# Kernel optimization log

Hardware: AMD Instinct MI355X
Metric: run time of the kernel (lower is better)

Reference implementation:

```python
import jax, jax.numpy as jnp
import numpy as np
import math

B, T, C = 4, 2048, 2048
HQ, HKV = 16, 4
HD = C // HQ          # 128
REP = HQ // HKV       # 4
EPS = 1e-6


def _rope_tables(seq_len, dim):
    inv_freq = 1.0 / (10000.0 ** (np.arange(0, dim, 2, dtype=np.float32) / dim))
    t = np.arange(seq_len, dtype=np.float32)
    freqs = np.einsum('i,j->ij', t, inv_freq)  # [T, dim/2]
    return jnp.asarray(np.cos(freqs)), jnp.asarray(np.sin(freqs))


def setup_inputs() -> dict:
    key = jax.random.key(0)
    ks = jax.random.split(key, 10)
    s = 0.02
    cos, sin = _rope_tables(T, HD)
    return {
        'x': jax.random.normal(ks[0], (B, T, C), jnp.float32),
        'Wq': jax.random.normal(ks[1], (C, C), jnp.float32) * s,
        'bq': jnp.zeros((C,), jnp.float32),
        'Wk': jax.random.normal(ks[2], (HD * HKV, C), jnp.float32) * s,
        'bk': jnp.zeros((HD * HKV,), jnp.float32),
        'Wv': jax.random.normal(ks[3], (HD * HKV, C), jnp.float32) * s,
        'bv': jnp.zeros((HD * HKV,), jnp.float32),
        'qn_w': jnp.ones((HD,), jnp.float32),
        'kn_w': jnp.ones((HD,), jnp.float32),
        'Wg': jax.random.normal(ks[4], (HD, HD), jnp.float32) * s,
        'bg': jnp.zeros((HD,), jnp.float32),
        'Wo': jax.random.normal(ks[5], (C, C), jnp.float32) * s,
        'bo': jnp.zeros((C,), jnp.float32),
        'cos': cos,
        'sin': sin,
    }


def _apply_rope(x, cos, sin):
    # x: [B,T,H,HD]; cos/sin: [T,HD/2]
    c = cos[None, :, None, :]
    s = sin[None, :, None, :]
    x1, x2 = x[..., ::2], x[..., 1::2]
    return jnp.concatenate([x1 * c - x2 * s, x1 * s + x2 * c], axis=-1)


def _rmsnorm(x, w):
    norm = jnp.mean(x * x, axis=-1, keepdims=True)
    return w * (x * jax.lax.rsqrt(norm + EPS))


def reference(x, Wq, bq, Wk, bk, Wv, bv, qn_w, kn_w, Wg, bg, Wo, bo, cos, sin):
    Bsz, Tlen, _ = x.shape
    q = (x @ Wq.T + bq).reshape(Bsz, Tlen, HQ, HD)
    k = (x @ Wk.T + bk).reshape(Bsz, Tlen, HKV, HD)
    v = (x @ Wv.T + bv).reshape(Bsz, Tlen, HKV, HD)

    q = _rmsnorm(_apply_rope(q, cos, sin), qn_w)
    k = _rmsnorm(_apply_rope(k, cos, sin), kn_w)

    # GQA without materializing repeated K/V: group q heads [B,T,HKV,REP,HD]
    # (repeat_interleave on kv-head dim matches this grouping exactly)
    q5 = q.reshape(Bsz, Tlen, HKV, REP, HD)
    scores = jnp.einsum('btkrd,bskd->bkrts', q5, k) / math.sqrt(HD)

    causal = jnp.tril(jnp.ones((Tlen, Tlen), bool))
    scores = jnp.where(causal, scores, -jnp.inf)
    probs = jax.nn.softmax(scores, axis=-1)

    out = jnp.einsum('bkrts,bskd->btkrd', probs, v).reshape(Bsz, Tlen, HQ, HD)
    gate = jax.nn.sigmoid(out @ Wg.T + bg)
    out = (out * gate).reshape(Bsz, Tlen, C)
    return out @ Wo.T + bo
```

## Files before the change

### kernel.cpp

```cpp
#include <hip/hip_runtime.h>
#include <hip/hip_bf16.h>
#include <math.h>

typedef __attribute__((ext_vector_type(8))) __bf16 bf16x8;
typedef __attribute__((ext_vector_type(4))) float f32x4;

__device__ __forceinline__ void stage16(const void* g, void* l) {
#if __has_builtin(__builtin_amdgcn_global_load_lds)
  __builtin_amdgcn_global_load_lds(
      (const __attribute__((address_space(1))) void*)g,
      (__attribute__((address_space(3))) void*)l, 16, 0, 0);
#else
  *(int4*)l = *(const int4*)g;
#endif
}

__device__ __forceinline__ float sigmoidf_(float x) {
  return 1.0f / (1.0f + __expf(-x));
}

__device__ __forceinline__ void f2b4(const float* __restrict__ s, __bf16* __restrict__ d) {
  float4 v = *(const float4*)s;
  union { __bf16 h[4]; int2 p; } u;
  u.h[0] = (__bf16)v.x; u.h[1] = (__bf16)v.y;
  u.h[2] = (__bf16)v.z; u.h[3] = (__bf16)v.w;
  *(int2*)d = u.p;
}

__global__ __launch_bounds__(256) void prep(const float* __restrict__ x,
                                            const float* __restrict__ Wq,
                                            const float* __restrict__ Wk,
                                            const float* __restrict__ Wv,
                                            const float* __restrict__ Wo,
                                            const float* __restrict__ Wg,
                                            const float* __restrict__ bq,
                                            const float* __restrict__ bk,
                                            const float* __restrict__ bv,
                                            __bf16* __restrict__ XB,
                                            __bf16* __restrict__ WQKVb,
                                            __bf16* __restrict__ WOb,
                                            __bf16* __restrict__ WGb,
                                            float* __restrict__ BQKV) {
  int c = blockIdx.x * 256 + threadIdx.x;
  if (c >= 6820608) return;
  if (c < 4194304) {
    f2b4(x + (size_t)c * 4, XB + (size_t)c * 4);
  } else if (c < 5242880) {
    int e = (c - 4194304) * 4;  f2b4(Wq + e, WQKVb + e);
  } else if (c < 5505024) {
    int e = (c - 5242880) * 4;  f2b4(Wk + e, WQKVb + 4194304 + e);
  } else if (c < 5767168) {
    int e = (c - 5505024) * 4;  f2b4(Wv + e, WQKVb + 5242880 + e);
  } else if (c < 6815744) {
    int e = (c - 5767168) * 4;  f2b4(Wo + e, WOb + e);
  } else if (c < 6819840) {
    int e = (c - 6815744) * 4;  f2b4(Wg + e, WGb + e);
  } else {
    int e = (c - 6819840) * 4;
    float4 v;
    if (e < 2048)      v = *(const float4*)(bq + e);
    else if (e < 2560) v = *(const float4*)(bk + (e - 2048));
    else               v = *(const float4*)(bv + (e - 2560));
    *(float4*)(BQKV + e) = v;
  }
}

template <typename OutT>
__global__ __launch_bounds__(512, 1) void gemm256(const __bf16* __restrict__ A,
                                                  const __bf16* __restrict__ Bm,
                                                  const float* __restrict__ bias,
                                                  OutT* __restrict__ C,
                                                  int M, int N, int K, int gx) {
  __shared__ __align__(16) __bf16 Sm[2][2][2][128 * 64];
  const int tid = threadIdx.x, lane = tid & 63, wid = tid >> 6;
  const int wm = wid >> 2, wn = wid & 3;
  const int r = lane & 15, g4 = lane >> 4;
  const int nwg = gridDim.x, qx = nwg >> 3;
  const int wg = (blockIdx.x & 7) * qx + (blockIdx.x >> 3);
  const int m0 = (wg / gx) * 256, n0 = (wg % gx) * 256;

  f32x4 acc[8][4] = {};
  const int NT = K >> 6;

#define STAGE_HALF(buf, which, half, kt)                                          \
  {                                                                               \
    const __bf16* sp_ = (which) ? Bm : A;                                         \
    const int base_ = ((which) ? n0 : m0) + (half) * 128;                         \
    const int k0_ = (kt) << 6;                                                    \
    __bf16* dp_ = &Sm[buf][which][half][0];                                       \
    _Pragma("unroll") for (int i_ = 0; i_ < 2; ++i_) {                            \
      int c_ = i_ * 512 + tid;                                                    \
      int row_ = c_ >> 3, slot_ = c_ & 7;                                         \
      stage16(sp_ + (size_t)(base_ + row_) * K + k0_ + ((slot_ ^ (row_ & 7)) << 3), \
              dp_ + c_ * 8);                                                      \
    }                                                                             \
  }
#define LDSW(base, row, kk) \
  (*(const bf16x8*)&(base)[(row) * 64 + ((((kk) * 4 + g4) ^ ((row) & 7)) << 3)])

  STAGE_HALF(0, 0, 0, 0) STAGE_HALF(0, 0, 1, 0) STAGE_HALF(0, 1, 0, 0) STAGE_HALF(0, 1, 1, 0)

  const int brow = (wn & 1) * 64;
  bf16x8 af[4][2], bfr[2][2];

  for (int kt = 0; kt < NT; ++kt) {
    const int cur = kt & 1, nxt = cur ^ 1;
    const bool more = (kt + 1) < NT;
    const __bf16* Ah = &Sm[cur][0][wm][0];
    const __bf16* Bh = &Sm[cur][1][wn >> 1][0];

    if (more) STAGE_HALF(nxt, 0, 0, kt + 1)
    if (more) { asm volatile("s_waitcnt vmcnt(2)" ::: "memory"); }
    else      { asm volatile("s_waitcnt vmcnt(0)" ::: "memory"); }
    __builtin_amdgcn_s_barrier();
    asm volatile("" ::: "memory");
#pragma unroll
    for (int m = 0; m < 4; ++m)
#pragma unroll
      for (int kk = 0; kk < 2; ++kk) af[m][kk] = LDSW(Ah, m * 16 + r, kk);
#pragma unroll
    for (int n = 0; n < 2; ++n)
#pragma unroll
      for (int kk = 0; kk < 2; ++kk) bfr[n][kk] = LDSW(Bh, brow + n * 16 + r, kk);
    asm volatile("s_waitcnt lgkmcnt(0)" ::: "memory");
    __builtin_amdgcn_sched_barrier(0);
    __builtin_amdgcn_s_setprio(1);
#pragma unroll
    for (int m = 0; m < 4; ++m)
#pragma unroll
      for (int n = 0; n < 2; ++n)
#pragma unroll
        for (int kk = 0; kk < 2; ++kk)
          acc[m][n] = __builtin_amdgcn_mfma_f32_16x16x32_bf16(af[m][kk], bfr[n][kk],
                                                              acc[m][n], 0, 0, 0);
    __builtin_amdgcn_s_setprio(0);
    __builtin_amdgcn_s_barrier();

#pragma unroll
    for (int n = 0; n < 2; ++n)
#pragma unroll
      for (int kk = 0; kk < 2; ++kk) bfr[n][kk] = LDSW(Bh, brow + (2 + n) * 16 + r, kk);
    if (more) STAGE_HALF(nxt, 0, 1, kt + 1)
    asm volatile("s_waitcnt lgkmcnt(0)" ::: "memory");
    __builtin_amdgcn_sched_barrier(0);
    __builtin_amdgcn_s_setprio(1);
#pragma unroll
    for (int m = 0; m < 4; ++m)
#pragma unroll
      for (int n = 0; n < 2; ++n)
#pragma unroll
        for (int kk = 0; kk < 2; ++kk)
          acc[m][2 + n] = __builtin_amdgcn_mfma_f32_16x16x32_bf16(af[m][kk], bfr[n][kk],
                                                                  acc[m][2 + n], 0, 0, 0);
    __builtin_amdgcn_s_setprio(0);
    __builtin_amdgcn_s_barrier();

#pragma unroll
    for (int m = 0; m < 4; ++m)
#pragma unroll
      for (int kk = 0; kk < 2; ++kk) af[m][kk] = LDSW(Ah, (4 + m) * 16 + r, kk);
#pragma unroll
    for (int n = 0; n < 2; ++n)
#pragma unroll
      for (int kk = 0; kk < 2; ++kk) bfr[n][kk] = LDSW(Bh, brow + n * 16 + r, kk);
    if (more) STAGE_HALF(nxt, 1, 0, kt + 1)
    asm volatile("s_waitcnt lgkmcnt(0)" ::: "memory");
    __builtin_amdgcn_sched_barrier(0);
    __builtin_amdgcn_s_setprio(1);
#pragma unroll
    for (int m = 0; m < 4; ++m)
#pragma unroll
      for (int n = 0; n < 2; ++n)
#pragma unroll
        for (int kk = 0; kk < 2; ++kk)
          acc[4 + m][n] = __builtin_amdgcn_mfma_f32_16x16x32_bf16(af[m][kk], bfr[n][kk],
                                                                  acc[4 + m][n], 0, 0, 0);
    __builtin_amdgcn_s_setprio(0);
    __builtin_amdgcn_s_barrier();

#pragma unroll
    for (int n = 0; n < 2; ++n)
#pragma unroll
      for (int kk = 0; kk < 2; ++kk) bfr[n][kk] = LDSW(Bh, brow + (2 + n) * 16 + r, kk);
    if (more) STAGE_HALF(nxt, 1, 1, kt + 1)
    asm volatile("s_waitcnt lgkmcnt(0)" ::: "memory");
    __builtin_amdgcn_sched_barrier(0);
    __builtin_amdgcn_s_setprio(1);
#pragma unroll
    for (int m = 0; m < 4; ++m)
#pragma unroll
      for (int n = 0; n < 2; ++n)
#pragma unroll
        for (int kk = 0; kk < 2; ++kk)
          acc[4 + m][2 + n] = __builtin_amdgcn_mfma_f32_16x16x32_bf16(af[m][kk], bfr[n][kk],
                                                                      acc[4 + m][2 + n], 0, 0, 0);
    __builtin_amdgcn_s_setprio(0);
    __builtin_amdgcn_s_barrier();
  }

  const int rq = lane >> 4;
#pragma unroll
  for (int m = 0; m < 8; ++m)
#pragma unroll
    for (int n = 0; n < 4; ++n) {
      int col = n0 + wn * 64 + n * 16 + r;
      float bv = bias ? bias[col] : 0.0f;
#pragma unroll
      for (int j = 0; j < 4; ++j) {
        int row = m0 + wm * 128 + m * 16 + rq * 4 + j;
        C[(size_t)row * N + col] = (OutT)(acc[m][n][j] + bv);
      }
    }
#undef STAGE_HALF
#undef LDSW
}

__global__ __launch_bounds__(512, 1) void gemm128(const __bf16* __restrict__ A,
                                                  const __bf16* __restrict__ Bm,
                                                  const float* __restrict__ bias,
                                                  __bf16* __restrict__ C,
                                                  int M, int N, int K, int gx) {
  __shared__ __align__(16) __bf16 Sm[2][3][128 * 64];
  const int tid = threadIdx.x, lane = tid & 63, wid = tid >> 6;
  const int wm = wid >> 2, wn = wid & 3;
  const int r = lane & 15, g4 = lane >> 4;
  const int nwg = gridDim.x, qx = nwg >> 3;
  const int wg = (blockIdx.x & 7) * qx + (blockIdx.x >> 3);
  const int m0 = (wg / gx) * 128, n0 = (wg % gx) * 256;

  f32x4 acc[4][4] = {};
  const int NT = K >> 6;

#define STAGE_SEG(buf, seg, sp, rowbase, kt)                                        \
  {                                                                                 \
    __bf16* dp_ = &Sm[buf][seg][0];                                                 \
    const int k0_ = (kt) << 6;                                                      \
    _Pragma("unroll") for (int i_ = 0; i_ < 2; ++i_) {                              \
      int c_ = i_ * 512 + tid;                                                      \
      int row_ = c_ >> 3, slot_ = c_ & 7;                                           \
      stage16((sp) + (size_t)((rowbase) + row_) * K + k0_ + ((slot_ ^ (row_ & 7)) << 3), \
              dp_ + c_ * 8);                                                        \
    }                                                                               \
  }
#define LDSW(base, row, kk) \
  (*(const bf16x8*)&(base)[(row) * 64 + ((((kk) * 4 + g4) ^ ((row) & 7)) << 3)])

  STAGE_SEG(0, 0, A, m0, 0) STAGE_SEG(0, 1, Bm, n0, 0) STAGE_SEG(0, 2, Bm, n0 + 128, 0)

  const int bseg = 1 + (wn >> 1);
  const int brow = (wn & 1) * 64;
  bf16x8 af[4][2], bfr[2][2];

  for (int kt = 0; kt < NT; ++kt) {
    const int cur = kt & 1, nxt = cur ^ 1;
    const bool more = (kt + 1) < NT;
    const __bf16* Ah = &Sm[cur][0][0];
    const __bf16* Bh = &Sm[cur][bseg][0];

    if (more) { STAGE_SEG(nxt, 0, A, m0, kt + 1) STAGE_SEG(nxt, 1, Bm, n0, kt + 1) }
    if (more) { asm volatile("s_waitcnt vmcnt(4)" ::: "memory"); }
    else      { asm volatile("s_waitcnt vmcnt(0)" ::: "memory"); }
    __builtin_amdgcn_s_barrier();
    asm volatile("" ::: "memory");
#pragma unroll
    for (int m = 0; m < 4; ++m)
#pragma unroll
      for (int kk = 0; kk < 2; ++kk) af[m][kk] = LDSW(Ah, wm * 64 + m * 16 + r, kk);
#pragma unroll
    for (int n = 0; n < 2; ++n)
#pragma unroll
      for (int kk = 0; kk < 2; ++kk) bfr[n][kk] = LDSW(Bh, brow + n * 16 + r, kk);
    asm volatile("s_waitcnt lgkmcnt(0)" ::: "memory");
    __builtin_amdgcn_sched_barrier(0);
    __builtin_amdgcn_s_setprio(1);
#pragma unroll
    for (int m = 0; m < 4; ++m)
#pragma unroll
      for (int n = 0; n < 2; ++n)
#pragma unroll
        for (int kk = 0; kk < 2; ++kk)
          acc[m][n] = __builtin_amdgcn_mfma_f32_16x16x32_bf16(af[m][kk], bfr[n][kk],
                                                              acc[m][n], 0, 0, 0);
    __builtin_amdgcn_s_setprio(0);
    __builtin_amdgcn_s_barrier();

#pragma unroll
    for (int n = 0; n < 2; ++n)
#pragma unroll
      for (int kk = 0; kk < 2; ++kk) bfr[n][kk] = LDSW(Bh, brow + (2 + n) * 16 + r, kk);
    if (more) STAGE_SEG(nxt, 2, Bm, n0 + 128, kt + 1)
    asm volatile("s_waitcnt lgkmcnt(0)" ::: "memory");
    __builtin_amdgcn_sched_barrier(0);
    __builtin_amdgcn_s_setprio(1);
#pragma unroll
    for (int m = 0; m < 4; ++m)
#pragma unroll
      for (int n = 0; n < 2; ++n)
#pragma unroll
        for (int kk = 0; kk < 2; ++kk)
          acc[m][2 + n] = __builtin_amdgcn_mfma_f32_16x16x32_bf16(af[m][kk], bfr[n][kk],
                                                                  acc[m][2 + n], 0, 0, 0);
    __builtin_amdgcn_s_setprio(0);
    __builtin_amdgcn_s_barrier();
  }

  const int rq = lane >> 4;
#pragma unroll
  for (int m = 0; m < 4; ++m)
#pragma unroll
    for (int n = 0; n < 4; ++n) {
      int col = n0 + wn * 64 + n * 16 + r;
      float bv = bias ? bias[col] : 0.0f;
#pragma unroll
      for (int j = 0; j < 4; ++j) {
        int row = m0 + wm * 64 + m * 16 + rq * 4 + j;
        C[(size_t)row * N + col] = (__bf16)(acc[m][n][j] + bv);
      }
    }
#undef STAGE_SEG
#undef LDSW
}

__global__ __launch_bounds__(256) void rope_vt(const __bf16* __restrict__ Y,
                                               const float* __restrict__ cosT,
                                               const float* __restrict__ sinT,
                                               const float* __restrict__ qn,
                                               const float* __restrict__ kn,
                                               __bf16* __restrict__ qat,
                                               __bf16* __restrict__ kat,
                                               __bf16* __restrict__ VT) {
  __shared__ __bf16 tile[32][66];
  if (blockIdx.x < 8192) {
    const int tok = blockIdx.x;
    const int b = tok >> 11, t = tok & 2047;
    const int wv = threadIdx.x >> 6, l = threadIdx.x & 63;
    const __bf16* row = Y + (size_t)tok * 3072;
    const float c = cosT[t * 64 + l], s = sinT[t * 64 + l];
    const float QS = 0.08838834764831845f * 1.4426950408889634f;
#pragma unroll
    for (int i = 0; i < 5; ++i) {
      const int h = wv + i * 4;
      const bool isq = h < 16;
      const int base = isq ? h * 128 : 2048 + (h - 16) * 128;
      union { uint32_t u; __bf16 h2[2]; } p;
      p.u = *(const uint32_t*)(row + base + 2 * l);
      float x1 = (float)p.h2[0], x2 = (float)p.h2[1];
      float v1 = x1 * c - x2 * s;
      float v2 = x1 * s + x2 * c;
      float ss = v1 * v1 + v2 * v2;
#pragma unroll
      for (int o = 32; o >= 1; o >>= 1) ss += __shfl_xor(ss, o, 64);
      float rms = rsqrtf(ss * (1.0f / 128.0f) + 1e-6f);
      if (isq) rms *= QS;
      float w1 = isq ? qn[l] : kn[l];
      float w2 = isq ? qn[64 + l] : kn[64 + l];
      size_t ob = isq ? (((size_t)b * 16 + h) * 2048 + t) * 128
                      : (((size_t)b * 4 + (h - 16)) * 2048 + t) * 128;
      __bf16* dst = isq ? qat : kat;
      dst[ob + l] = (__bf16)(w1 * v1 * rms);
      dst[ob + 64 + l] = (__bf16)(w2 * v2 * rms);
    }
  } else {
    const int i = blockIdx.x - 8192;
    const int t0 = (i & 31) * 64;
    const int d0 = ((i >> 5) & 3) * 32;
    const int bh = i >> 7;
    const int b = bh >> 2, hv = bh & 3;
    const __bf16* src = Y + (size_t)b * 2048 * 3072 + 2560 + hv * 128 + d0;
    const int dd = threadIdx.x & 31, tt = threadIdx.x >> 5;
#pragma unroll
    for (int p = 0; p < 8; ++p) {
      int t = tt + p * 8;
      tile[dd][t] = src[(size_t)(t0 + t) * 3072 + dd];
    }
    __syncthreads();
    __bf16* dst = VT + ((size_t)bh * 128 + d0) * 2048 + t0;
    const int oc = threadIdx.x & 63, orr = threadIdx.x >> 6;
#pragma unroll
    for (int p = 0; p < 8; ++p) {
      int d = orr + p * 4;
      dst[(size_t)d * 2048 + oc] = tile[d][oc];
    }
  }
}

__global__ __launch_bounds__(512, 4) void attn9(const __bf16* __restrict__ Q,
                                                const __bf16* __restrict__ Kg,
                                                const __bf16* __restrict__ VTg,
                                                __bf16* __restrict__ ab) {
  __shared__ __align__(16) __bf16 Kt[2][64 * 128];
  __shared__ __align__(16) __bf16 Vt[2][128 * 64];
  __shared__ __align__(16) __bf16 Ps[8 * 16 * 64];
  const int tid = threadIdx.x, lane = tid & 63, wv = tid >> 6;
  const int L = blockIdx.x;
  const int xcd = L & 7, slot = L >> 3;
  const int group = xcd * 2 + (slot >> 5);
  const int idx = slot & 31;
  const int b = group >> 2, hkv = group & 3;
  const int hq = hkv * 4 + (idx >> 3);
  const int p = idx & 7;
  const __bf16* qp = Q + ((size_t)b * 16 + hq) * 2048 * 128;
  const __bf16* kp = Kg + ((size_t)b * 4 + hkv) * 2048 * 128;
  const __bf16* vp = VTg + ((size_t)b * 4 + hkv) * 128 * 2048;
  const int r = lane & 15, g4 = lane >> 4, ks = g4 * 8;

  bf16x8 vone;
#pragma unroll
  for (int e = 0; e < 8; ++e) vone[e] = (__bf16)1.0f;

#define STAGE_TILE(bi, kv0)                                                  \
  {                                                                          \
    __bf16* Kb = &Kt[bi][0];                                                 \
    __bf16* Vb = &Vt[bi][0];                                                 \
    _Pragma("unroll") for (int i = 0; i < 2; ++i) {                          \
      int c = i * 512 + tid;                                                 \
      int row = c >> 4, slot_ = c & 15;                                      \
      int gco = ((slot_ ^ (row & 7)) << 3);                                  \
      stage16(kp + (size_t)((kv0) + row) * 128 + gco, &Kb[c * 8]);           \
    }                                                                        \
    _Pragma("unroll") for (int i = 0; i < 2; ++i) {                          \
      int c = i * 512 + tid;                                                 \
      int row = c >> 3, slot_ = c & 7;                                       \
      int gco = ((slot_ ^ (row & 7)) << 3);                                  \
      stage16(vp + (size_t)row * 2048 + (kv0) + gco, &Vb[c * 8]);            \
    }                                                                        \
  }

  for (int half = 0; half < 2; ++half) {
    const int qt = half == 0 ? (15 - p) : p;
    const int q0 = qt * 128 + wv * 16;

    bf16x8 qf[4];
#pragma unroll
    for (int kk = 0; kk < 4; ++kk)
      qf[kk] = *(const bf16x8*)(qp + (size_t)(q0 + r) * 128 + kk * 32 + ks);

    f32x4 Of[8] = {};
    f32x4 Lacc = {};
    float mrow[4] = {-1e30f, -1e30f, -1e30f, -1e30f};

    const int nt = 2 * qt + 2;
    STAGE_TILE(0, 0);
    int cur = 0;
    for (int t = 0; t < nt; ++t) {
      const int kv0 = t * 64;
      if (t + 1 < nt) {
        STAGE_TILE(cur ^ 1, (t + 1) * 64);
        asm volatile("s_waitcnt vmcnt(4)" ::: "memory");
      } else {
        asm volatile("s_waitcnt vmcnt(0)" ::: "memory");
      }
      __builtin_amdgcn_s_barrier();

      const __bf16* Kb = &Kt[cur][0];
      const __bf16* Vb = &Vt[cur][0];

      f32x4 s[4];
      __builtin_amdgcn_s_setprio(1);
#pragma unroll
      for (int kj = 0; kj < 4; ++kj) {
        f32x4 sa = {};
        int krow = kj * 16 + r;
#pragma unroll
        for (int kk = 0; kk < 4; ++kk) {
          int slot_ = (kk * 4 + g4) ^ (r & 7);
          bf16x8 kf = *(const bf16x8*)&Kb[krow * 128 + slot_ * 8];
          sa = __builtin_amdgcn_mfma_f32_16x16x32_bf16(qf[kk], kf, sa, 0, 0, 0);
        }
        s[kj] = sa;
      }
      __builtin_amdgcn_s_setprio(0);
      if (kv0 + 63 > q0) {
#pragma unroll
        for (int kj = 0; kj < 4; ++kj)
#pragma unroll
          for (int j = 0; j < 4; ++j) {
            int kv = kv0 + kj * 16 + r;
            int qrow = q0 + g4 * 4 + j;
            if (kv > qrow) s[kj][j] = -1e30f;
          }
      }
      float tm[4];
#pragma unroll
      for (int j = 0; j < 4; ++j)
        tm[j] = fmaxf(fmaxf(s[0][j], s[1][j]), fmaxf(s[2][j], s[3][j]));
      bool need = (tm[0] > mrow[0] + 8.0f) | (tm[1] > mrow[1] + 8.0f) |
                  (tm[2] > mrow[2] + 8.0f) | (tm[3] > mrow[3] + 8.0f);
      if (__any(need)) {
#pragma unroll
        for (int o = 8; o >= 1; o >>= 1)
#pragma unroll
          for (int j = 0; j < 4; ++j) tm[j] = fmaxf(tm[j], __shfl_xor(tm[j], o, 64));
#pragma unroll
        for (int j = 0; j < 4; ++j) {
          float mn = fmaxf(mrow[j], tm[j]);
          float corr = exp2f(mrow[j] - mn);
          mrow[j] = mn;
          Lacc[j] *= corr;
#pragma unroll
          for (int f = 0; f < 8; ++f) Of[f][j] *= corr;
        }
      }
#pragma unroll
      for (int kj = 0; kj < 4; ++kj)
#pragma unroll
        for (int j = 0; j < 4; ++j) s[kj][j] = exp2f(s[kj][j] - mrow[j]);

      __bf16* pw = &Ps[wv * 16 * 64];
#pragma unroll
      for (int kj = 0; kj < 4; ++kj)
#pragma unroll
        for (int j = 0; j < 4; ++j) {
          int qr = g4 * 4 + j;
          int kvl = kj * 16 + r;
          int sl = (kvl >> 3) ^ (qr & 7);
          pw[qr * 64 + sl * 8 + (kvl & 7)] = (__bf16)s[kj][j];
        }
      __builtin_amdgcn_s_setprio(1);
#pragma unroll
      for (int kvj = 0; kvj < 2; ++kvj) {
        int sl = (kvj * 4 + g4) ^ (r & 7);
        bf16x8 pa = *(const bf16x8*)&pw[r * 64 + sl * 8];
        Lacc = __builtin_amdgcn_mfma_f32_16x16x32_bf16(pa, vone, Lacc, 0, 0, 0);
#pragma unroll
        for (int dn = 0; dn < 8; ++dn) {
          bf16x8 vb = *(const bf16x8*)&Vb[(dn * 16 + r) * 64 + sl * 8];
          Of[dn] = __builtin_amdgcn_mfma_f32_16x16x32_bf16(pa, vb, Of[dn], 0, 0, 0);
        }
      }
      __builtin_amdgcn_s_setprio(0);
      __builtin_amdgcn_s_barrier();
      cur ^= 1;
    }

    float inv[4];
#pragma unroll
    for (int j = 0; j < 4; ++j) inv[j] = 1.0f / Lacc[j];
#pragma unroll
    for (int dn = 0; dn < 8; ++dn)
#pragma unroll
      for (int j = 0; j < 4; ++j) {
        int row = q0 + g4 * 4 + j;
        int d = dn * 16 + r;
        ab[(((size_t)b * 2048 + row) * 16 + hq) * 128 + d] = (__bf16)(Of[dn][j] * inv[j]);
      }
  }
#undef STAGE_TILE
}

__global__ __launch_bounds__(256) void gate_fused(const __bf16* __restrict__ a,
                                                  const __bf16* __restrict__ WgB,
                                                  const float* __restrict__ bg,
                                                  __bf16* __restrict__ og) {
  __shared__ __align__(16) __bf16 Wl[128 * 128];
  const int tid = threadIdx.x, lane = tid & 63, wv = tid >> 6;
  const int r = lane & 15, g4 = lane >> 4, ks = g4 * 8;
#pragma unroll
  for (int i = 0; i < 8; ++i) {
    int c = i * 256 + tid;
    int row = c >> 4, slot = c & 15;
    *(bf16x8*)&Wl[row * 128 + ((slot ^ (row & 7)) << 3)] =
        *(const bf16x8*)&WgB[row * 128 + slot * 8];
  }
  __syncthreads();
  const size_t r0 = (size_t)blockIdx.x * 64 + wv * 16;
  bf16x8 af[4];
#pragma unroll
  for (int kk = 0; kk < 4; ++kk)
    af[kk] = *(const bf16x8*)(a + (r0 + r) * 128 + kk * 32 + ks);
  f32x4 acc[8] = {};
#pragma unroll
  for (int dn = 0; dn < 8; ++dn) {
    int row = dn * 16 + r;
#pragma unroll
    for (int kk = 0; kk < 4; ++kk) {
      bf16x8 bf_ = *(const bf16x8*)&Wl[row * 128 + (((kk * 4 + g4) ^ (row & 7)) << 3)];
      acc[dn] = __builtin_amdgcn_mfma_f32_16x16x32_bf16(af[kk], bf_, acc[dn], 0, 0, 0);
    }
  }
#pragma unroll
  for (int dn = 0; dn < 8; ++dn) {
    float bgv = bg[dn * 16 + r];
#pragma unroll
    for (int j = 0; j < 4; ++j) {
      size_t row = r0 + g4 * 4 + j;
      int col = dn * 16 + r;
      float gv = sigmoidf_(acc[dn][j] + bgv);
      float av = (float)a[row * 128 + col];
      og[row * 128 + col] = (__bf16)(av * gv);
    }
  }
}

extern "C" void kernel_launch(void* const* d_in, const int* in_sizes, int n_in,
                              void* d_out, int out_size, void* d_ws, size_t ws_size,
                              hipStream_t stream) {
  const float* x    = (const float*)d_in[0];
  const float* Wq   = (const float*)d_in[1];
  const float* bq   = (const float*)d_in[2];
  const float* Wk   = (const float*)d_in[3];
  const float* bk   = (const float*)d_in[4];
  const float* Wv   = (const float*)d_in[5];
  const float* bv   = (const float*)d_in[6];
  const float* qn   = (const float*)d_in[7];
  const float* kn   = (const float*)d_in[8];
  const float* Wg   = (const float*)d_in[9];
  const float* bg   = (const float*)d_in[10];
  const float* Wo   = (const float*)d_in[11];
  const float* bo   = (const float*)d_in[12];
  const float* cosT = (const float*)d_in[13];
  const float* sinT = (const float*)d_in[14];

  char* ws = (char*)d_ws;
  constexpr size_t OFF_WQKV = 0;
  constexpr size_t OFF_WO   = OFF_WQKV + 3072ull * 2048 * 2;
  constexpr size_t OFF_WG   = OFF_WO + 2048ull * 2048 * 2;
  constexpr size_t OFF_BQKV = OFF_WG + 128ull * 128 * 2;
  constexpr size_t OFF_XB   = OFF_BQKV + 16384;
  constexpr size_t OFF_Y    = OFF_XB + 8192ull * 2048 * 2;
  constexpr size_t OFF_QAT  = OFF_Y + 8192ull * 3072 * 2;
  constexpr size_t OFF_KAT  = OFF_QAT + 4ull * 16 * 2048 * 128 * 2;
  constexpr size_t OFF_VT   = OFF_KAT + 4ull * 4 * 2048 * 128 * 2;
  constexpr size_t OFF_AB   = OFF_VT + 4ull * 4 * 2048 * 128 * 2;

  __bf16* WQKVb = (__bf16*)(ws + OFF_WQKV);
  __bf16* WOb   = (__bf16*)(ws + OFF_WO);
  __bf16* WGb   = (__bf16*)(ws + OFF_WG);
  float*  BQKV  = (float*)(ws + OFF_BQKV);
  __bf16* XB    = (__bf16*)(ws + OFF_XB);
  __bf16* Y     = (__bf16*)(ws + OFF_Y);
  __bf16* QAT   = (__bf16*)(ws + OFF_QAT);
  __bf16* KAT   = (__bf16*)(ws + OFF_KAT);
  __bf16* VT    = (__bf16*)(ws + OFF_VT);
  __bf16* ABuf  = (__bf16*)(ws + OFF_AB);
  __bf16* OGB   = (__bf16*)(ws + OFF_XB);

  prep<<<26643, 256, 0, stream>>>(x, Wq, Wk, Wv, Wo, Wg, bq, bk, bv,
                                  XB, WQKVb, WOb, WGb, BQKV);

  gemm128<<<768, 512, 0, stream>>>(XB, WQKVb, BQKV, Y, 8192, 3072, 2048, 12);

  rope_vt<<<10240, 256, 0, stream>>>(Y, cosT, sinT, qn, kn, QAT, KAT, VT);

  attn9<<<512, 512, 0, stream>>>(QAT, KAT, VT, ABuf);

  gate_fused<<<2048, 256, 0, stream>>>(ABuf, WGb, bg, OGB);

  gemm256<float><<<256, 512, 0, stream>>>(OGB, WOb, bo, (float*)d_out, 8192, 2048, 2048, 8);
}
```

Baseline: 387.5 us.

## Finer-grained GEMM staging/MFMA interleave and split attention softmax with PV

In the QKV projection GEMM, the k-loop is now split into four MFMA phases of one 16-column B fragment each. The next-tile B staging loads are spread across these phases, and the mid-iteration barrier is dropped, so global-to-LDS traffic overlaps more compute with less synchronisation. The vmcnt wait is tightened so only the newest A segment stays in flight. In the attention kernel, exp2 and the P write-out now run in two halves, each followed by its PV MFMA chunk, so exponentials can overlap with matrix work. The risks are register-pressure changes and compiler scheduling that may not realise the intended overlap.

After: 389.9 us. About the same (+0.6%).

```diff
diff --git a/kernel.cpp b/kernel.cpp
--- a/kernel.cpp
+++ b/kernel.cpp
@@ -244,12 +244,21 @@
   }
 #define LDSW(base, row, kk) \
   (*(const bf16x8*)&(base)[(row) * 64 + ((((kk) * 4 + g4) ^ ((row) & 7)) << 3)])
+#define MFMA8(nq)                                                                   \
+  asm volatile("s_waitcnt lgkmcnt(0)" ::: "memory");                                \
+  __builtin_amdgcn_sched_barrier(0);                                                \
+  __builtin_amdgcn_s_setprio(1);                                                    \
+  _Pragma("unroll") for (int m = 0; m < 4; ++m)                                     \
+    _Pragma("unroll") for (int kk = 0; kk < 2; ++kk)                                \
+      acc[m][nq] = __builtin_amdgcn_mfma_f32_16x16x32_bf16(af[m][kk], bfr[kk],      \
+                                                           acc[m][nq], 0, 0, 0);    \
+  __builtin_amdgcn_s_setprio(0);
 
   STAGE_SEG(0, 0, A, m0, 0) STAGE_SEG(0, 1, Bm, n0, 0) STAGE_SEG(0, 2, Bm, n0 + 128, 0)
 
   const int bseg = 1 + (wn >> 1);
   const int brow = (wn & 1) * 64;
-  bf16x8 af[4][2], bfr[2][2];
+  bf16x8 af[4][2], bfr[2];
 
   for (int kt = 0; kt < NT; ++kt) {
     const int cur = kt & 1, nxt = cur ^ 1;
@@ -257,8 +266,8 @@
     const __bf16* Ah = &Sm[cur][0][0];
     const __bf16* Bh = &Sm[cur][bseg][0];
 
-    if (more) { STAGE_SEG(nxt, 0, A, m0, kt + 1) STAGE_SEG(nxt, 1, Bm, n0, kt + 1) }
-    if (more) { asm volatile("s_waitcnt vmcnt(4)" ::: "memory"); }
+    if (more) { STAGE_SEG(nxt, 0, A, m0, kt + 1)
+                asm volatile("s_waitcnt vmcnt(2)" ::: "memory"); }
     else      { asm volatile("s_waitcnt vmcnt(0)" ::: "memory"); }
     __builtin_amdgcn_s_barrier();
     asm volatile("" ::: "memory");
@@ -267,40 +276,22 @@
 #pragma unroll
       for (int kk = 0; kk < 2; ++kk) af[m][kk] = LDSW(Ah, wm * 64 + m * 16 + r, kk);
 #pragma unroll
-    for (int n = 0; n < 2; ++n)
-#pragma unroll
-      for (int kk = 0; kk < 2; ++kk) bfr[n][kk] = LDSW(Bh, brow + n * 16 + r, kk);
-    asm volatile("s_waitcnt lgkmcnt(0)" ::: "memory");
-    __builtin_amdgcn_sched_barrier(0);
-    __builtin_amdgcn_s_setprio(1);
-#pragma unroll
-    for (int m = 0; m < 4; ++m)
-#pragma unroll
-      for (int n = 0; n < 2; ++n)
-#pragma unroll
-        for (int kk = 0; kk < 2; ++kk)
-          acc[m][n] = __builtin_amdgcn_mfma_f32_16x16x32_bf16(af[m][kk], bfr[n][kk],
-                                                              acc[m][n], 0, 0, 0);
-    __builtin_amdgcn_s_setprio(0);
-    __builtin_amdgcn_s_barrier();
-
-#pragma unroll
-    for (int n = 0; n < 2; ++n)
-#pragma unroll
-      for (int kk = 0; kk < 2; ++kk) bfr[n][kk] = LDSW(Bh, brow + (2 + n) * 16 + r, kk);
+    for (int kk = 0; kk < 2; ++kk) bfr[kk] = LDSW(Bh, brow + r, kk);
+    MFMA8(0)
+
+#pragma unroll
+    for (int kk = 0; kk < 2; ++kk) bfr[kk] = LDSW(Bh, brow + 16 + r, kk);
+    if (more) STAGE_SEG(nxt, 1, Bm, n0, kt + 1)
+    MFMA8(1)
+
+#pragma unroll
+    for (int kk = 0; kk < 2; ++kk) bfr[kk] = LDSW(Bh, brow + 32 + r, kk);
     if (more) STAGE_SEG(nxt, 2, Bm, n0 + 128, kt + 1)
-    asm volatile("s_waitcnt lgkmcnt(0)" ::: "memory");
-    __builtin_amdgcn_sched_barrier(0);
-    __builtin_amdgcn_s_setprio(1);
-#pragma unroll
-    for (int m = 0; m < 4; ++m)
-#pragma unroll
-      for (int n = 0; n < 2; ++n)
-#pragma unroll
-        for (int kk = 0; kk < 2; ++kk)
-          acc[m][2 + n] = __builtin_amdgcn_mfma_f32_16x16x32_bf16(af[m][kk], bfr[n][kk],
-                                                                  acc[m][2 + n], 0, 0, 0);
-    __builtin_amdgcn_s_setprio(0);
+    MFMA8(2)
+
+#pragma unroll
+    for (int kk = 0; kk < 2; ++kk) bfr[kk] = LDSW(Bh, brow + 48 + r, kk);
+    MFMA8(3)
     __builtin_amdgcn_s_barrier();
   }
 
@@ -319,6 +310,7 @@
     }
 #undef STAGE_SEG
 #undef LDSW
+#undef MFMA8
 }
 
 __global__ __launch_bounds__(256) void rope_vt(const __bf16* __restrict__ Y,
@@ -384,10 +376,10 @@
   }
 }
 
-__global__ __launch_bounds__(512, 4) void attn9(const __bf16* __restrict__ Q,
-                                                const __bf16* __restrict__ Kg,
-                                                const __bf16* __restrict__ VTg,
-                                                __bf16* __restrict__ ab) {
+__global__ __launch_bounds__(512, 4) void attn10(const __bf16* __restrict__ Q,
+                                                 const __bf16* __restrict__ Kg,
+                                                 const __bf16* __restrict__ VTg,
+                                                 __bf16* __restrict__ ab) {
   __shared__ __align__(16) __bf16 Kt[2][64 * 128];
   __shared__ __align__(16) __bf16 Vt[2][128 * 64];
   __shared__ __align__(16) __bf16 Ps[8 * 16 * 64];
@@ -425,6 +417,27 @@
       stage16(vp + (size_t)row * 2048 + (kv0) + gco, &Vb[c * 8]);            \
     }                                                                        \
   }
+#define SM_PAIR(k0)                                                          \
+  _Pragma("unroll") for (int kj = (k0); kj < (k0) + 2; ++kj)                 \
+    _Pragma("unroll") for (int j = 0; j < 4; ++j) {                          \
+      float pv = exp2f(s[kj][j] - mrow[j]);                                  \
+      int qr = g4 * 4 + j;                                                   \
+      int kvl = kj * 16 + r;                                                 \
+      int sl = (kvl >> 3) ^ (qr & 7);                                        \
+      pw[qr * 64 + sl * 8 + (kvl & 7)] = (__bf16)pv;                         \
+    }
+#define PV_CHUNK(kvj)                                                        \
+  {                                                                          \
+    int sl = ((kvj) * 4 + g4) ^ (r & 7);                                     \
+    bf16x8 pa = *(const bf16x8*)&pw[r * 64 + sl * 8];                        \
+    __builtin_amdgcn_s_setprio(1);                                           \
+    Lacc = __builtin_amdgcn_mfma_f32_16x16x32_bf16(pa, vone, Lacc, 0, 0, 0); \
+    _Pragma("unroll") for (int dn = 0; dn < 8; ++dn) {                       \
+      bf16x8 vb = *(const bf16x8*)&Vb[(dn * 16 + r) * 64 + sl * 8];          \
+      Of[dn] = __builtin_amdgcn_mfma_f32_16x16x32_bf16(pa, vb, Of[dn], 0, 0, 0); \
+    }                                                                        \
+    __builtin_amdgcn_s_setprio(0);                                           \
+  }
 
   for (int half = 0; half < 2; ++half) {
     const int qt = half == 0 ? (15 - p) : p;
@@ -501,34 +514,12 @@
           for (int f = 0; f < 8; ++f) Of[f][j] *= corr;
         }
       }
-#pragma unroll
-      for (int kj = 0; kj < 4; ++kj)
-#pragma unroll
-        for (int j = 0; j < 4; ++j) s[kj][j] = exp2f(s[kj][j] - mrow[j]);
 
       __bf16* pw = &Ps[wv * 16 * 64];
-#pragma unroll
-      for (int kj = 0; kj < 4; ++kj)
-#pragma unroll
-        for (int j = 0; j < 4; ++j) {
-          int qr = g4 * 4 + j;
-          int kvl = kj * 16 + r;
-          int sl = (kvl >> 3) ^ (qr & 7);
-          pw[qr * 64 + sl * 8 + (kvl & 7)] = (__bf16)s[kj][j];
-        }
-      __builtin_amdgcn_s_setprio(1);
-#pragma unroll
-      for (int kvj = 0; kvj < 2; ++kvj) {
-        int sl = (kvj * 4 + g4) ^ (r & 7);
-        bf16x8 pa = *(const bf16x8*)&pw[r * 64 + sl * 8];
-        Lacc = __builtin_amdgcn_mfma_f32_16x16x32_bf16(pa, vone, Lacc, 0, 0, 0);
-#pragma unroll
-        for (int dn = 0; dn < 8; ++dn) {
-          bf16x8 vb = *(const bf16x8*)&Vb[(dn * 16 + r) * 64 + sl * 8];
-          Of[dn] = __builtin_amdgcn_mfma_f32_16x16x32_bf16(pa, vb, Of[dn], 0, 0, 0);
-        }
-      }
-      __builtin_amdgcn_s_setprio(0);
+      SM_PAIR(0)
+      PV_CHUNK(0)
+      SM_PAIR(2)
+      PV_CHUNK(1)
       __builtin_amdgcn_s_barrier();
       cur ^= 1;
     }
@@ -546,6 +537,8 @@
       }
   }
 #undef STAGE_TILE
+#undef SM_PAIR
+#undef PV_CHUNK
 }
 
 __global__ __launch_bounds__(256) void gate_fused(const __bf16* __restrict__ a,
@@ -642,7 +635,7 @@
 
   rope_vt<<<10240, 256, 0, stream>>>(Y, cosT, sinT, qn, kn, QAT, KAT, VT);
 
-  attn9<<<512, 512, 0, stream>>>(QAT, KAT, VT, ABuf);
+  attn10<<<512, 512, 0, stream>>>(QAT, KAT, VT, ABuf);
 
   gate_fused<<<2048, 256, 0, stream>>>(ABuf, WGb, bg, OGB);
 
```
